# Kernel optimization log

Measured on AMD Instinct MI355X. Metric: run time of the kernel, lower is better.

Reference implementation:

```python
import jax, jax.numpy as jnp
import numpy as np
from jax.scipy.linalg import expm

M = 8          # number of mixture models
S = 4          # alphabet size (nucleotides)
N_LEAVES = 20  # taxa
K = 19         # internal nodes (caterpillar binary tree)
BATCH = 200000 # alignment sites


def _build_tree():
    # Caterpillar rooted binary tree: internal node n has children (leaf0, leaf1);
    # internal node n+j has children (internal n+j-1, leaf j+1). T[b, a] = branch length b->a.
    n, k = N_LEAVES, K
    N = n + k
    rng = np.random.default_rng(0)
    T = np.zeros((N, N), dtype=np.float32)
    T[0, n] = rng.uniform(0.05, 1.0)
    T[1, n] = rng.uniform(0.05, 1.0)
    for j in range(1, k):
        a = n + j
        T[a - 1, a] = rng.uniform(0.05, 1.0)
        T[j + 1, a] = rng.uniform(0.05, 1.0)
    return T


def setup_inputs() -> dict:
    key = jax.random.key(0)
    k1, k2 = jax.random.split(key, 2)
    X = jax.random.uniform(k1, (BATCH, N_LEAVES, S), dtype=jnp.float32)
    rates = jax.random.uniform(k2, (M, S * (S - 1) // 2), dtype=jnp.float32)
    pi_inv = jnp.full((M, S - 1), 1.0 / (np.sqrt(S) - 1.0), dtype=jnp.float32)
    rho = jnp.ones((M,), dtype=jnp.float32)
    T = _build_tree()  # numpy: tree structure is static config, not a traced tensor
    return {"X": X, "rates": rates, "pi_inv": pi_inv, "rho": rho, "T": T}


def _inv_stereographic_projection(y):
    ns = jnp.sum(y ** 2, axis=-1)
    return jnp.concatenate([2.0 * y, (ns - 1.0)[..., None]], axis=-1) / (ns + 1.0)[..., None]


def _rate_matrices(rates_sq, pi):
    # rates_sq: [M, s(s-1)/2], pi: [M, s] -> Q: [M, s, s]
    iu, ju = np.triu_indices(S, 1)
    Q = jnp.zeros((M, S, S), rates_sq.dtype).at[:, iu, ju].set(rates_sq)
    Q = Q + jnp.swapaxes(Q, 1, 2)                    # symmetrize
    Q = Q * pi[:, None, :]                           # stationary probabilities
    new_diag = -jnp.sum(Q, axis=2)                   # row sums -> diagonal
    ar = np.arange(S)
    Q = Q.at[:, ar, ar].set(new_diag)
    emut = jnp.maximum(-jnp.sum(pi * new_diag, axis=1), 1e-9)
    return Q / emut[:, None, None]                   # one expected mutation per unit time


def _forward(X, rates, pi_inv, rho, Tnp):
    n, k = N_LEAVES, K
    pi = _inv_stereographic_projection(pi_inv) ** 2          # [M, S]
    Q = _rate_matrices(rates ** 2, pi) * rho[:, None, None]  # [M, S, S]
    es, et = np.nonzero(Tnp)
    A = []  # per internal node: [BATCH, M, S] partial likelihoods
    for a in range(n, n + k):
        ch = es[et == a]
        t = jnp.asarray(Tnp[ch, a])                          # [C] branch lengths
        P = expm(t[:, None, None, None] * Q[None])           # [C, M, S, S] batched small expm
        parts = []
        for i, b in enumerate(ch):
            if b < n:
                parts.append(jnp.einsum('mcd,id->imc', P[i], X[:, b, :]))
            else:
                parts.append(jnp.einsum('mcd,imd->imc', P[i], A[b - n]))
        A.append(jnp.prod(jnp.stack(parts), axis=0))         # Felsenstein pruning product
    return jnp.einsum('imc,mc->im', A[-1], pi)               # [BATCH, M]


def reference(X, rates, pi_inv, rho, T):
    return _forward(X, rates, pi_inv, rho, np.asarray(T))
```

## Files before the change

kernel.cpp:

```cpp
#include <hip/hip_runtime.h>
#include <math.h>

#define MM 8
#define SS 4
#define NLEAF 20
#define KINT 19
#define NBR 38
#define P4 (NBR*MM*4)
#define PFLOATS (P4*4)
#define NNODE 39

typedef float v2f __attribute__((ext_vector_type(2)));
typedef float v4f __attribute__((ext_vector_type(4)));


__device__ __forceinline__ void mat4_mul(const double a[4][4], const double b[4][4], double c[4][4]) {
    #pragma unroll
    for (int i = 0; i < 4; i++)
        #pragma unroll
        for (int j = 0; j < 4; j++) {
            double s = 0.0;
            #pragma unroll
            for (int k = 0; k < 4; k++) s += a[i][k] * b[k][j];
            c[i][j] = s;
        }
}

__global__ void setup_kernel(const float* __restrict__ rates,
                             const float* __restrict__ pi_inv,
                             const float* __restrict__ rho,
                             const float* __restrict__ T,
                             float* __restrict__ ws)
{
    int tid = blockIdx.x * blockDim.x + threadIdx.x;
    if (tid >= NBR * MM) return;
    int m = tid & 7;
    int k = tid >> 3;

    double y0 = pi_inv[m*3+0], y1 = pi_inv[m*3+1], y2 = pi_inv[m*3+2];
    double ns  = y0*y0 + y1*y1 + y2*y2;
    double inv = 1.0 / (ns + 1.0);
    double p[4] = {2.0*y0*inv, 2.0*y1*inv, 2.0*y2*inv, (ns-1.0)*inv};
    #pragma unroll
    for (int i = 0; i < 4; i++) p[i] *= p[i];

    if (k == 0) {
        #pragma unroll
        for (int i = 0; i < 4; i++) ws[PFLOATS + m*4 + i] = (float)p[i];
    }

    double r[6];
    #pragma unroll
    for (int i = 0; i < 6; i++) { double v = rates[m*6+i]; r[i] = v*v; }
    double Q[4][4] = {};
    Q[0][1]=r[0]; Q[0][2]=r[1]; Q[0][3]=r[2]; Q[1][2]=r[3]; Q[1][3]=r[4]; Q[2][3]=r[5];
    #pragma unroll
    for (int i = 0; i < 4; i++)
        #pragma unroll
        for (int j = i+1; j < 4; j++) Q[j][i] = Q[i][j];
    #pragma unroll
    for (int i = 0; i < 4; i++)
        #pragma unroll
        for (int j = 0; j < 4; j++) Q[i][j] *= p[j];
    double emut = 0.0;
    #pragma unroll
    for (int i = 0; i < 4; i++) {
        double rs = 0.0;
        #pragma unroll
        for (int j = 0; j < 4; j++) if (j != i) rs += Q[i][j];
        Q[i][i] = -rs;
        emut += p[i] * rs;
    }
    emut = fmax(emut, 1e-9);
    double scq = (double)rho[m] / emut;

    double t;
    if      (k == 0) t = T[0*NNODE + NLEAF];
    else if (k == 1) t = T[1*NNODE + NLEAF];
    else {
        int j     = k >> 1;
        int node  = NLEAF + j;
        int child = (k & 1) ? (j + 1) : (NLEAF - 1 + j);
        t = T[child*NNODE + node];
    }

    double A[4][4];
    #pragma unroll
    for (int i = 0; i < 4; i++)
        #pragma unroll
        for (int j = 0; j < 4; j++) A[i][j] = Q[i][j] * scq * t;

    double nrm = 0.0;
    #pragma unroll
    for (int i = 0; i < 4; i++) {
        double rs = 0.0;
        #pragma unroll
        for (int j = 0; j < 4; j++) rs += fabs(A[i][j]);
        nrm = fmax(nrm, rs);
    }
    int s = 0;
    if (nrm > 0.0625) s = (int)ceil(log2(nrm * 16.0));
    if (s < 0) s = 0;
    if (s > 60) s = 60;
    double scl = ldexp(1.0, -s);
    double B[4][4];
    #pragma unroll
    for (int i = 0; i < 4; i++)
        #pragma unroll
        for (int j = 0; j < 4; j++) B[i][j] = A[i][j] * scl;

    double E[4][4];
    #pragma unroll
    for (int i = 0; i < 4; i++)
        #pragma unroll
        for (int j = 0; j < 4; j++) E[i][j] = (i == j) ? 1.0 : 0.0;
    for (int kk = 9; kk >= 1; --kk) {
        double Tm[4][4];
        mat4_mul(B, E, Tm);
        double ik = 1.0 / (double)kk;
        #pragma unroll
        for (int i = 0; i < 4; i++)
            #pragma unroll
            for (int j = 0; j < 4; j++) E[i][j] = ((i == j) ? 1.0 : 0.0) + Tm[i][j] * ik;
    }
    for (int q = 0; q < s; q++) {
        double Tm[4][4];
        mat4_mul(E, E, Tm);
        #pragma unroll
        for (int i = 0; i < 4; i++)
            #pragma unroll
            for (int j = 0; j < 4; j++) E[i][j] = Tm[i][j];
    }

    float* Pout = ws + (k*MM + m) * 16;
    #pragma unroll
    for (int d = 0; d < 4; d++)
        #pragma unroll
        for (int c = 0; c < 4; c++) Pout[d*4+c] = (float)E[c][d];
}


__device__ __forceinline__ void dotc(v4f c0, v4f c1, v4f c2, v4f c3,
                                     v2f s0, v2f s1, v2f s2, v2f s3,
                                     v2f& lo, v2f& hi)
{
    v2f l = (v2f){c0.x, c0.y} * s0;
    v2f h = (v2f){c0.z, c0.w} * s0;
    l = __builtin_elementwise_fma((v2f){c1.x, c1.y}, s1, l);
    h = __builtin_elementwise_fma((v2f){c1.z, c1.w}, s1, h);
    l = __builtin_elementwise_fma((v2f){c2.x, c2.y}, s2, l);
    h = __builtin_elementwise_fma((v2f){c2.z, c2.w}, s2, h);
    l = __builtin_elementwise_fma((v2f){c3.x, c3.y}, s3, l);
    h = __builtin_elementwise_fma((v2f){c3.z, c3.w}, s3, h);
    lo = l; hi = h;
}

__global__ __launch_bounds__(128) void phylo_kernel(const float* __restrict__ X,
                                                    const float* __restrict__ ws,
                                                    float* __restrict__ out,
                                                    int batch)
{
    __shared__ v4f Pl[P4 + MM];
    const v4f* w4 = (const v4f*)ws;
    for (int idx = threadIdx.x; idx < P4 + MM; idx += 128) Pl[idx] = w4[idx];
    __syncthreads();

    const int t  = threadIdx.x;
    const int i0 = blockIdx.x * 256 + t;
    const int i1 = i0 + 128;
    const size_t b0 = (size_t)(i0 < batch ? i0 : batch - 1) * 20;
    const size_t b1 = (size_t)(i1 < batch ? i1 : batch - 1) * 20;
    const v4f* X4 = (const v4f*)X;

    v2f alo[2][MM], ahi[2][MM];

    {
        v4f x00 = X4[b0+0], x01 = X4[b0+1];
        v4f x10 = X4[b1+0], x11 = X4[b1+1];
        v2f sA0={x00.x,x00.x}, sA1={x00.y,x00.y}, sA2={x00.z,x00.z}, sA3={x00.w,x00.w};
        v2f sB0={x01.x,x01.x}, sB1={x01.y,x01.y}, sB2={x01.z,x01.z}, sB3={x01.w,x01.w};
        v2f sC0={x10.x,x10.x}, sC1={x10.y,x10.y}, sC2={x10.z,x10.z}, sC3={x10.w,x10.w};
        v2f sD0={x11.x,x11.x}, sD1={x11.y,x11.y}, sD2={x11.z,x11.z}, sD3={x11.w,x11.w};
        #pragma unroll
        for (int m = 0; m < MM; m++) {
            const v4f* PA = &Pl[(0*MM + m) * 4];
            const v4f* PB = &Pl[(1*MM + m) * 4];
            v4f a0=PA[0], a1=PA[1], a2=PA[2], a3=PA[3];
            v4f e0=PB[0], e1=PB[1], e2=PB[2], e3=PB[3];
            v2f tl, th, ul, uh;
            dotc(a0,a1,a2,a3, sA0,sA1,sA2,sA3, tl, th);
            dotc(e0,e1,e2,e3, sB0,sB1,sB2,sB3, ul, uh);
            alo[0][m] = tl*ul; ahi[0][m] = th*uh;
            dotc(a0,a1,a2,a3, sC0,sC1,sC2,sC3, tl, th);
            dotc(e0,e1,e2,e3, sD0,sD1,sD2,sD3, ul, uh);
            alo[1][m] = tl*ul; ahi[1][m] = th*uh;
        }
    }

    v4f xl0 = X4[b0 + 2], xl1 = X4[b1 + 2];
    #pragma unroll 1
    for (int j = 1; j < KINT; j++) {
        v4f nx0 = xl0, nx1 = xl1;
        if (j < KINT - 1) { nx0 = X4[b0 + j + 2]; nx1 = X4[b1 + j + 2]; }

        const v4f* PI = &Pl[(2*j) * MM * 4];
        const v4f* PL = PI + MM * 4;

        v2f x0s0={xl0.x,xl0.x}, x0s1={xl0.y,xl0.y}, x0s2={xl0.z,xl0.z}, x0s3={xl0.w,xl0.w};
        v2f x1s0={xl1.x,xl1.x}, x1s1={xl1.y,xl1.y}, x1s2={xl1.z,xl1.z}, x1s3={xl1.w,xl1.w};

        #pragma unroll
        for (int m = 0; m < MM; m++) {
            v4f ci0=PI[m*4+0], ci1=PI[m*4+1], ci2=PI[m*4+2], ci3=PI[m*4+3];
            v4f cl0=PL[m*4+0], cl1=PL[m*4+1], cl2=PL[m*4+2], cl3=PL[m*4+3];
            v2f tl, th, ul, uh;
            dotc(ci0,ci1,ci2,ci3,
                 (v2f){alo[0][m].x, alo[0][m].x}, (v2f){alo[0][m].y, alo[0][m].y},
                 (v2f){ahi[0][m].x, ahi[0][m].x}, (v2f){ahi[0][m].y, ahi[0][m].y},
                 tl, th);
            dotc(cl0,cl1,cl2,cl3, x0s0,x0s1,x0s2,x0s3, ul, uh);
            alo[0][m] = tl*ul; ahi[0][m] = th*uh;
            dotc(ci0,ci1,ci2,ci3,
                 (v2f){alo[1][m].x, alo[1][m].x}, (v2f){alo[1][m].y, alo[1][m].y},
                 (v2f){ahi[1][m].x, ahi[1][m].x}, (v2f){ahi[1][m].y, ahi[1][m].y},
                 tl, th);
            dotc(cl0,cl1,cl2,cl3, x1s0,x1s1,x1s2,x1s3, ul, uh);
            alo[1][m] = tl*ul; ahi[1][m] = th*uh;
        }
        xl0 = nx0; xl1 = nx1;
    }

    float r0[MM], r1[MM];
    #pragma unroll
    for (int m = 0; m < MM; m++) {
        v4f pim = Pl[P4 + m];
        v2f plo = (v2f){pim.x, pim.y}, phi = (v2f){pim.z, pim.w};
        v2f s0 = __builtin_elementwise_fma(ahi[0][m], phi, alo[0][m] * plo);
        v2f s1 = __builtin_elementwise_fma(ahi[1][m], phi, alo[1][m] * plo);
        r0[m] = s0.x + s0.y;
        r1[m] = s1.x + s1.y;
    }
    v4f* o4 = (v4f*)out;
    if (i0 < batch) {
        o4[(size_t)i0*2 + 0] = (v4f){r0[0], r0[1], r0[2], r0[3]};
        o4[(size_t)i0*2 + 1] = (v4f){r0[4], r0[5], r0[6], r0[7]};
    }
    if (i1 < batch) {
        o4[(size_t)i1*2 + 0] = (v4f){r1[0], r1[1], r1[2], r1[3]};
        o4[(size_t)i1*2 + 1] = (v4f){r1[4], r1[5], r1[6], r1[7]};
    }
}


extern "C" void kernel_launch(void* const* d_in, const int* in_sizes, int n_in,
                              void* d_out, int out_size, void* d_ws, size_t ws_size,
                              hipStream_t stream)
{
    const float* X      = (const float*)d_in[0];
    const float* rates  = (const float*)d_in[1];
    const float* pi_inv = (const float*)d_in[2];
    const float* rho    = (const float*)d_in[3];
    const float* T      = (const float*)d_in[4];
    float* out = (float*)d_out;
    float* ws  = (float*)d_ws;

    int batch = in_sizes[0] / (NLEAF * SS);

    hipLaunchKernelGGL(setup_kernel, dim3(1), dim3(320), 0, stream,
                       rates, pi_inv, rho, T, ws);

    int grid = (batch + 255) / 256;
    hipLaunchKernelGGL(phylo_kernel, dim3(grid), dim3(128), 0, stream,
                       X, ws, out, batch);
}
```

Measured before the change: 131.4 us.

## Split mixture models across warps with 8 sites per thread

Reorganizes the pruning kernel so each wavefront handles a single mixture model m, with each lane processing 8 sites. Threads once carried all 8 models for 2 sites. This lets the per-model transition matrices for a step be held in registers across 8 sites, which cuts LDS traffic, and it double-buffers the leaf loads. The trade-off is that every leaf vector X is now read by all 8 model waves (through cache), and output stores become scalar and strided by model.

After: 218.2 us. 66.0% more time.

```diff
diff --git a/kernel.cpp b/kernel.cpp
--- a/kernel.cpp
+++ b/kernel.cpp
@@ -9,6 +9,8 @@
 #define P4 (NBR*MM*4)
 #define PFLOATS (P4*4)
 #define NNODE 39
+#define SPT 8
+#define SPB 512
 
 typedef float v2f __attribute__((ext_vector_type(2)));
 typedef float v4f __attribute__((ext_vector_type(4)));
@@ -140,114 +142,109 @@
 }
 
 
-__device__ __forceinline__ void dotc(v4f c0, v4f c1, v4f c2, v4f c3,
-                                     v2f s0, v2f s1, v2f s2, v2f s3,
-                                     v2f& lo, v2f& hi)
-{
-    v2f l = (v2f){c0.x, c0.y} * s0;
-    v2f h = (v2f){c0.z, c0.w} * s0;
-    l = __builtin_elementwise_fma((v2f){c1.x, c1.y}, s1, l);
-    h = __builtin_elementwise_fma((v2f){c1.z, c1.w}, s1, h);
-    l = __builtin_elementwise_fma((v2f){c2.x, c2.y}, s2, l);
-    h = __builtin_elementwise_fma((v2f){c2.z, c2.w}, s2, h);
-    l = __builtin_elementwise_fma((v2f){c3.x, c3.y}, s3, l);
-    h = __builtin_elementwise_fma((v2f){c3.z, c3.w}, s3, h);
+#define SHUF(v,a,b) __builtin_shufflevector((v),(v),(a),(b))
+
+__device__ __forceinline__ void matvx(const v4f& c0, const v4f& c1, const v4f& c2, const v4f& c3,
+                                      const v4f& x, v2f& lo, v2f& hi)
+{
+    v2f l = SHUF(c0,0,1) * SHUF(x,0,0);
+    v2f h = SHUF(c0,2,3) * SHUF(x,0,0);
+    l = __builtin_elementwise_fma(SHUF(c1,0,1), SHUF(x,1,1), l);
+    h = __builtin_elementwise_fma(SHUF(c1,2,3), SHUF(x,1,1), h);
+    l = __builtin_elementwise_fma(SHUF(c2,0,1), SHUF(x,2,2), l);
+    h = __builtin_elementwise_fma(SHUF(c2,2,3), SHUF(x,2,2), h);
+    l = __builtin_elementwise_fma(SHUF(c3,0,1), SHUF(x,3,3), l);
+    h = __builtin_elementwise_fma(SHUF(c3,2,3), SHUF(x,3,3), h);
     lo = l; hi = h;
 }
 
-__global__ __launch_bounds__(128) void phylo_kernel(const float* __restrict__ X,
+__device__ __forceinline__ void matvs(const v4f& c0, const v4f& c1, const v4f& c2, const v4f& c3,
+                                      v2f alo, v2f ahi, v2f& lo, v2f& hi)
+{
+    v2f l = SHUF(c0,0,1) * SHUF(alo,0,0);
+    v2f h = SHUF(c0,2,3) * SHUF(alo,0,0);
+    l = __builtin_elementwise_fma(SHUF(c1,0,1), SHUF(alo,1,1), l);
+    h = __builtin_elementwise_fma(SHUF(c1,2,3), SHUF(alo,1,1), h);
+    l = __builtin_elementwise_fma(SHUF(c2,0,1), SHUF(ahi,0,0), l);
+    h = __builtin_elementwise_fma(SHUF(c2,2,3), SHUF(ahi,0,0), h);
+    l = __builtin_elementwise_fma(SHUF(c3,0,1), SHUF(ahi,1,1), l);
+    h = __builtin_elementwise_fma(SHUF(c3,2,3), SHUF(ahi,1,1), h);
+    lo = l; hi = h;
+}
+
+#define LOADX(B, LEAF) { _Pragma("unroll") for (int k = 0; k < SPT; k++) B[k] = xp[k][(LEAF)]; }
+
+#define STEP(J, XB) { \
+    const v4f* PI = &Pl[((2*(J))*MM + m)*4]; \
+    const v4f* PL = PI + MM*4; \
+    v4f ci0=PI[0], ci1=PI[1], ci2=PI[2], ci3=PI[3]; \
+    v4f cl0=PL[0], cl1=PL[1], cl2=PL[2], cl3=PL[3]; \
+    _Pragma("unroll") for (int k = 0; k < SPT; k++) { \
+        v2f tl, th, ul, uh; \
+        matvs(ci0,ci1,ci2,ci3, lo[k], hi[k], tl, th); \
+        matvx(cl0,cl1,cl2,cl3, XB[k], ul, uh); \
+        lo[k] = tl*ul; hi[k] = th*uh; \
+    } }
+
+__global__ __launch_bounds__(512) void phylo_kernel(const float* __restrict__ X,
                                                     const float* __restrict__ ws,
                                                     float* __restrict__ out,
                                                     int batch)
 {
     __shared__ v4f Pl[P4 + MM];
     const v4f* w4 = (const v4f*)ws;
-    for (int idx = threadIdx.x; idx < P4 + MM; idx += 128) Pl[idx] = w4[idx];
+    for (int idx = threadIdx.x; idx < P4 + MM; idx += 512) Pl[idx] = w4[idx];
     __syncthreads();
 
-    const int t  = threadIdx.x;
-    const int i0 = blockIdx.x * 256 + t;
-    const int i1 = i0 + 128;
-    const size_t b0 = (size_t)(i0 < batch ? i0 : batch - 1) * 20;
-    const size_t b1 = (size_t)(i1 < batch ? i1 : batch - 1) * 20;
-    const v4f* X4 = (const v4f*)X;
-
-    v2f alo[2][MM], ahi[2][MM];
-
+    const int lane = threadIdx.x & 63;
+    const int m    = threadIdx.x >> 6;
+    const int siteBase = blockIdx.x * SPB;
+
+    const v4f* xp[SPT];
+    #pragma unroll
+    for (int k = 0; k < SPT; k++) {
+        int s = siteBase + lane + 64*k;
+        if (s >= batch) s = batch - 1;
+        xp[k] = (const v4f*)X + (size_t)s * 20;
+    }
+
+    v2f lo[SPT], hi[SPT];
+
+    v4f XA[SPT], XB[SPT];
+    LOADX(XA, 0);
+    LOADX(XB, 1);
     {
-        v4f x00 = X4[b0+0], x01 = X4[b0+1];
-        v4f x10 = X4[b1+0], x11 = X4[b1+1];
-        v2f sA0={x00.x,x00.x}, sA1={x00.y,x00.y}, sA2={x00.z,x00.z}, sA3={x00.w,x00.w};
-        v2f sB0={x01.x,x01.x}, sB1={x01.y,x01.y}, sB2={x01.z,x01.z}, sB3={x01.w,x01.w};
-        v2f sC0={x10.x,x10.x}, sC1={x10.y,x10.y}, sC2={x10.z,x10.z}, sC3={x10.w,x10.w};
-        v2f sD0={x11.x,x11.x}, sD1={x11.y,x11.y}, sD2={x11.z,x11.z}, sD3={x11.w,x11.w};
-        #pragma unroll
-        for (int m = 0; m < MM; m++) {
-            const v4f* PA = &Pl[(0*MM + m) * 4];
-            const v4f* PB = &Pl[(1*MM + m) * 4];
-            v4f a0=PA[0], a1=PA[1], a2=PA[2], a3=PA[3];
-            v4f e0=PB[0], e1=PB[1], e2=PB[2], e3=PB[3];
+        const v4f* P0 = &Pl[(0*MM + m)*4];
+        const v4f* P1 = P0 + MM*4;
+        v4f a0=P0[0], a1=P0[1], a2=P0[2], a3=P0[3];
+        v4f e0=P1[0], e1=P1[1], e2=P1[2], e3=P1[3];
+        #pragma unroll
+        for (int k = 0; k < SPT; k++) {
             v2f tl, th, ul, uh;
-            dotc(a0,a1,a2,a3, sA0,sA1,sA2,sA3, tl, th);
-            dotc(e0,e1,e2,e3, sB0,sB1,sB2,sB3, ul, uh);
-            alo[0][m] = tl*ul; ahi[0][m] = th*uh;
-            dotc(a0,a1,a2,a3, sC0,sC1,sC2,sC3, tl, th);
-            dotc(e0,e1,e2,e3, sD0,sD1,sD2,sD3, ul, uh);
-            alo[1][m] = tl*ul; ahi[1][m] = th*uh;
+            matvx(a0,a1,a2,a3, XA[k], tl, th);
+            matvx(e0,e1,e2,e3, XB[k], ul, uh);
+            lo[k] = tl*ul; hi[k] = th*uh;
         }
     }
 
-    v4f xl0 = X4[b0 + 2], xl1 = X4[b1 + 2];
+    LOADX(XA, 2);
     #pragma unroll 1
-    for (int j = 1; j < KINT; j++) {
-        v4f nx0 = xl0, nx1 = xl1;
-        if (j < KINT - 1) { nx0 = X4[b0 + j + 2]; nx1 = X4[b1 + j + 2]; }
-
-        const v4f* PI = &Pl[(2*j) * MM * 4];
-        const v4f* PL = PI + MM * 4;
-
-        v2f x0s0={xl0.x,xl0.x}, x0s1={xl0.y,xl0.y}, x0s2={xl0.z,xl0.z}, x0s3={xl0.w,xl0.w};
-        v2f x1s0={xl1.x,xl1.x}, x1s1={xl1.y,xl1.y}, x1s2={xl1.z,xl1.z}, x1s3={xl1.w,xl1.w};
-
-        #pragma unroll
-        for (int m = 0; m < MM; m++) {
-            v4f ci0=PI[m*4+0], ci1=PI[m*4+1], ci2=PI[m*4+2], ci3=PI[m*4+3];
-            v4f cl0=PL[m*4+0], cl1=PL[m*4+1], cl2=PL[m*4+2], cl3=PL[m*4+3];
-            v2f tl, th, ul, uh;
-            dotc(ci0,ci1,ci2,ci3,
-                 (v2f){alo[0][m].x, alo[0][m].x}, (v2f){alo[0][m].y, alo[0][m].y},
-                 (v2f){ahi[0][m].x, ahi[0][m].x}, (v2f){ahi[0][m].y, ahi[0][m].y},
-                 tl, th);
-            dotc(cl0,cl1,cl2,cl3, x0s0,x0s1,x0s2,x0s3, ul, uh);
-            alo[0][m] = tl*ul; ahi[0][m] = th*uh;
-            dotc(ci0,ci1,ci2,ci3,
-                 (v2f){alo[1][m].x, alo[1][m].x}, (v2f){alo[1][m].y, alo[1][m].y},
-                 (v2f){ahi[1][m].x, ahi[1][m].x}, (v2f){ahi[1][m].y, ahi[1][m].y},
-                 tl, th);
-            dotc(cl0,cl1,cl2,cl3, x1s0,x1s1,x1s2,x1s3, ul, uh);
-            alo[1][m] = tl*ul; ahi[1][m] = th*uh;
-        }
-        xl0 = nx0; xl1 = nx1;
-    }
-
-    float r0[MM], r1[MM];
-    #pragma unroll
-    for (int m = 0; m < MM; m++) {
-        v4f pim = Pl[P4 + m];
-        v2f plo = (v2f){pim.x, pim.y}, phi = (v2f){pim.z, pim.w};
-        v2f s0 = __builtin_elementwise_fma(ahi[0][m], phi, alo[0][m] * plo);
-        v2f s1 = __builtin_elementwise_fma(ahi[1][m], phi, alo[1][m] * plo);
-        r0[m] = s0.x + s0.y;
-        r1[m] = s1.x + s1.y;
-    }
-    v4f* o4 = (v4f*)out;
-    if (i0 < batch) {
-        o4[(size_t)i0*2 + 0] = (v4f){r0[0], r0[1], r0[2], r0[3]};
-        o4[(size_t)i0*2 + 1] = (v4f){r0[4], r0[5], r0[6], r0[7]};
-    }
-    if (i1 < batch) {
-        o4[(size_t)i1*2 + 0] = (v4f){r1[0], r1[1], r1[2], r1[3]};
-        o4[(size_t)i1*2 + 1] = (v4f){r1[4], r1[5], r1[6], r1[7]};
+    for (int jj = 0; jj < 9; ++jj) {
+        int jA = 1 + 2*jj;
+        LOADX(XB, 3 + 2*jj);
+        STEP(jA, XA);
+        if (jj < 8) LOADX(XA, 4 + 2*jj);
+        STEP(jA + 1, XB);
+    }
+
+    v4f pim = Pl[P4 + m];
+    v2f plo = SHUF(pim,0,1), phi = SHUF(pim,2,3);
+    #pragma unroll
+    for (int k = 0; k < SPT; k++) {
+        v2f s = __builtin_elementwise_fma(hi[k], phi, lo[k]*plo);
+        float r = s.x + s.y;
+        int st = siteBase + lane + 64*k;
+        if (st < batch) out[(size_t)st*MM + m] = r;
     }
 }
 
@@ -269,7 +266,7 @@
     hipLaunchKernelGGL(setup_kernel, dim3(1), dim3(320), 0, stream,
                        rates, pi_inv, rho, T, ws);
 
-    int grid = (batch + 255) / 256;
-    hipLaunchKernelGGL(phylo_kernel, dim3(grid), dim3(128), 0, stream,
+    int grid = (batch + SPB - 1) / SPB;
+    hipLaunchKernelGGL(phylo_kernel, dim3(grid), dim3(512), 0, stream,
                        X, ws, out, batch);
 }
```
